# Kernel tuning notes

Hardware: AMD Instinct MI355X
Metric: run time of the kernel (lower is better)

## Reference

```python
import jax, jax.numpy as jnp
import numpy as np

N = 50000      # nodes
E = 800000     # edges (avg degree 16)
IN = 256       # in_feats
H = 256        # hidden_size
HEADS = 4
DH = H // HEADS  # 64
SCALE = np.sqrt(DH).astype(np.float32)


def _lin_init(k, fan_in, fan_out):
    s = 1.0 / np.sqrt(fan_in)
    k1, k2 = jax.random.split(k)
    W = jax.random.uniform(k1, (fan_in, fan_out), jnp.float32, -s, s)
    b = jax.random.uniform(k2, (fan_out,), jnp.float32, -s, s)
    return W, b


def setup_inputs() -> dict:
    key = jax.random.key(0)
    ks = jax.random.split(key, 20)
    d = {}
    d["features"] = jax.random.normal(ks[0], (N, IN), jnp.float32)
    d["src"] = jax.random.randint(ks[1], (E,), 0, N)
    d["dst"] = jax.random.randint(ks[2], (E,), 0, N)
    d["edge_types"] = jax.random.randint(ks[3], (E,), 0, 4)
    d["Wm"], d["bm"] = _lin_init(ks[4], IN, H)
    i = 5
    for l in (1, 2, 3):
        for nm in ("Q", "K", "V"):
            d[f"W{nm}{l}"], d[f"b{nm}{l}"] = _lin_init(ks[i], H, H)
            i += 1
    d["W1"], d["b1"] = _lin_init(ks[i], 3 * H, 2 * H); i += 1
    d["W2"], d["b2"] = _lin_init(ks[i], 2 * H, H); i += 1
    d["W3"], d["b3"] = _lin_init(ks[i], H, 1)
    return d


def _norms(src, dst):
    # DGL GraphConv norm='both': src normalized by out-degree, dst by in-degree
    ones = jnp.ones((E,), jnp.float32)
    deg_out = jax.ops.segment_sum(ones, src, num_segments=N)
    deg_in = jax.ops.segment_sum(ones, dst, num_segments=N)
    ns = jnp.where(deg_out > 0, deg_out ** -0.5, 0.0)[:, None]  # [N,1]
    nd = jnp.where(deg_in > 0, deg_in ** -0.5, 0.0)[:, None]
    return ns, nd


def _gcn(x, W, b, src, dst, ns, nd):
    # h = D_in^{-1/2} A D_out^{-1/2} x W + b
    m = (x * ns)[src]                                   # [E,H] gather
    agg = jax.ops.segment_sum(m, dst, num_segments=N)   # [N,H] scatter-sum
    return (agg * nd) @ W + b


def _attn(x, WQ, bQ, WK, bK, WV, bV, src, dst, ns, nd):
    Q = jax.nn.relu(_gcn(x, WQ, bQ, src, dst, ns, nd)).reshape(N, HEADS, DH)
    K = jax.nn.relu(_gcn(x, WK, bK, src, dst, ns, nd)).reshape(N, HEADS, DH)
    V = jax.nn.relu(_gcn(x, WV, bV, src, dst, ns, nd)).reshape(N, HEADS, DH)
    # edge scores: src K dot dst Q, scaled exp with clamp
    score = jnp.exp(jnp.clip((K[src] * Q[dst]).sum(-1) / SCALE, -10.0, 10.0))  # [E,HEADS]
    wV = jax.ops.segment_sum(V[src] * score[:, :, None], dst, num_segments=N)  # [N,HEADS,DH]
    z = jax.ops.segment_sum(score, dst, num_segments=N)                        # [N,HEADS]
    return (wV / (z[:, :, None] + 1e-6)).reshape(N, H)


def reference(features, src, dst, edge_types, Wm, bm,
              WQ1, bQ1, WK1, bK1, WV1, bV1,
              WQ2, bQ2, WK2, bK2, WV2, bV2,
              WQ3, bQ3, WK3, bK3, WV3, bV3,
              W1, b1, W2, b2, W3, b3):
    ns, nd = _norms(src, dst)
    x = jax.nn.relu(features @ Wm + bm)
    x1 = _attn(x, WQ1, bQ1, WK1, bK1, WV1, bV1, src, dst, ns, nd)
    x2 = _attn(x1, WQ2, bQ2, WK2, bK2, WV2, bV2, src, dst, ns, nd)
    x3 = _attn(x2, WQ3, bQ3, WK3, bK3, WV3, bV3, src, dst, ns, nd)
    x = jnp.concatenate((x1, x2, x3), axis=1)          # [N, 3H]
    x = jax.nn.relu(x @ W1 + b1)
    x = jax.nn.relu(x @ W2 + b2)
    x = (x @ W3 + b3)[:, 0]
    return jax.nn.sigmoid(x)
```

## Files before the change

kernel.cpp:

```cpp
#include <hip/hip_runtime.h>
#include <stdint.h>

#define NN 50000
#define NE 800000
#define NBLK 196

typedef float f32x4 __attribute__((ext_vector_type(4)));
typedef short s16x8 __attribute__((ext_vector_type(8)));

__device__ __forceinline__ float bf2f(unsigned short u) {
    union { unsigned int i; float f; } v; v.i = ((unsigned int)u) << 16; return v.f;
}
__device__ __forceinline__ unsigned short f2bf(float x) {
    union { float f; unsigned int i; } v; v.f = x;
    unsigned int r = v.i + 0x7FFFu + ((v.i >> 16) & 1u);
    return (unsigned short)(r >> 16);
}


__global__ void k_deg(const int* __restrict__ src, const int* __restrict__ dst,
                      int* __restrict__ dego, int* __restrict__ degi) {
    int e = blockIdx.x * 256 + threadIdx.x;
    if (e < NE) {
        atomicAdd(&dego[src[e]], 1);
        atomicAdd(&degi[dst[e]], 1);
    }
}

__global__ void k_norm(const int* __restrict__ dego, const int* __restrict__ degi,
                       float* __restrict__ ns, float* __restrict__ nd) {
    int i = blockIdx.x * 256 + threadIdx.x;
    if (i < NN) {
        ns[i] = dego[i] > 0 ? rsqrtf((float)dego[i]) : 0.f;
        nd[i] = degi[i] > 0 ? rsqrtf((float)degi[i]) : 0.f;
    }
}

__global__ void k_scanA(const int* __restrict__ deg, int* __restrict__ incl,
                        int* __restrict__ bsum) {
    __shared__ int sm[256];
    int t = threadIdx.x, i = blockIdx.x * 256 + t;
    int v = (i < NN) ? deg[i] : 0;
    sm[t] = v;
    __syncthreads();
#pragma unroll
    for (int off = 1; off < 256; off <<= 1) {
        int tv = (t >= off) ? sm[t - off] : 0;
        __syncthreads();
        sm[t] += tv;
        __syncthreads();
    }
    if (i < NN) incl[i] = sm[t];
    if (t == 255) bsum[blockIdx.x] = sm[255];
}

__global__ void k_scanB(const int* __restrict__ bsum, int* __restrict__ boff,
                        int* __restrict__ row_ptr) {
    __shared__ int sm[256];
    int t = threadIdx.x;
    int v = (t < NBLK) ? bsum[t] : 0;
    sm[t] = v;
    __syncthreads();
#pragma unroll
    for (int off = 1; off < 256; off <<= 1) {
        int tv = (t >= off) ? sm[t - off] : 0;
        __syncthreads();
        sm[t] += tv;
        __syncthreads();
    }
    if (t < NBLK) boff[t] = sm[t] - v;
    if (t == 255) row_ptr[NN] = sm[255];
}

__global__ void k_scanC(const int* __restrict__ deg, const int* __restrict__ incl,
                        const int* __restrict__ boff, int* __restrict__ row_ptr,
                        int* __restrict__ cursor) {
    int i = blockIdx.x * 256 + threadIdx.x;
    if (i < NN) {
        int ex = boff[blockIdx.x] + incl[i] - deg[i];
        row_ptr[i] = ex;
        cursor[i] = ex;
    }
}

__global__ void k_fill(const int* __restrict__ src, const int* __restrict__ dst,
                       const float* __restrict__ ns,
                       int* __restrict__ cursor, int* __restrict__ col_src,
                       float* __restrict__ ewt) {
    int e = blockIdx.x * 256 + threadIdx.x;
    if (e < NE) {
        int s = src[e];
        int slot = atomicAdd(&cursor[dst[e]], 1);
        col_src[slot] = s;
        ewt[slot] = ns[s];
    }
}

__global__ void k_wsplit(const float* __restrict__ W, unsigned short* __restrict__ hi,
                         unsigned short* __restrict__ lo, int K, int Ncols) {
    int idx = blockIdx.x * 256 + threadIdx.x;
    if (idx < K * Ncols) {
        int n = idx / K, k = idx - n * K;
        float w = W[(size_t)k * Ncols + n];
        unsigned short h = f2bf(w);
        hi[idx] = h;
        lo[idx] = f2bf(w - bf2f(h));
    }
}

struct QkvPtrs {
    const float* w[9];
    unsigned short* h[3];
    unsigned short* l[3];
};

__global__ void k_wsplit9(QkvPtrs P) {
    int m = blockIdx.y;
    int layer = m / 3, which = m - layer * 3;
    int idx = blockIdx.x * 256 + threadIdx.x;
    int n = idx >> 8, k = idx & 255;
    float w = P.w[m][(size_t)k * 256 + n];
    unsigned short h = f2bf(w);
    size_t o = (size_t)(which * 256 + n) * 256 + k;
    P.h[layer][o] = h;
    P.l[layer][o] = f2bf(w - bf2f(h));
}

struct BiasPtrs { const float* b[9]; float* dst; };

__global__ void k_bcat(BiasPtrs P) {
    int m = blockIdx.x;
    int layer = m / 3, which = m - layer * 3;
    int t = threadIdx.x;
    P.dst[layer * 768 + which * 256 + t] = P.b[m][t];
}


__global__ void k_prop(const float* __restrict__ x, int ldx,
                       const int* __restrict__ row_ptr, const int* __restrict__ col_src,
                       const float* __restrict__ ewt, const float* __restrict__ ndv,
                       float* __restrict__ y) {
    int w = (int)((blockIdx.x * 256 + threadIdx.x) >> 6);
    if (w >= NN) return;
    int lane = threadIdx.x & 63;
    int c = lane * 4;
    float a0 = 0, a1 = 0, a2 = 0, a3 = 0;
    int e0 = row_ptr[w], e1 = row_ptr[w + 1];
    int sv = (e0 < e1) ? col_src[e0] : 0;
    for (int p = e0; p < e1; ++p) {
        int sn = (p + 1 < e1) ? col_src[p + 1] : 0;
        float wv = ewt[p];
        const float4 xv = *(const float4*)(x + (size_t)sv * ldx + c);
        a0 += wv * xv.x; a1 += wv * xv.y; a2 += wv * xv.z; a3 += wv * xv.w;
        sv = sn;
    }
    float sc = ndv[w];
    float4 o; o.x = a0 * sc; o.y = a1 * sc; o.z = a2 * sc; o.w = a3 * sc;
    *(float4*)(y + (size_t)w * 256 + c) = o;
}


__global__ void k_attn(const float* __restrict__ Qbuf, const unsigned short* __restrict__ KV,
                       const int* __restrict__ row_ptr, const int* __restrict__ col_src,
                       float* __restrict__ xo) {
    int w = (int)((blockIdx.x * 256 + threadIdx.x) >> 6);
    if (w >= NN) return;
    int lane = threadIdx.x & 63;
    int c = lane * 4;
    const float4 q = *(const float4*)(Qbuf + (size_t)w * 256 + c);
    float v0 = 0, v1 = 0, v2 = 0, v3 = 0, z = 0;
    int e0 = row_ptr[w], e1 = row_ptr[w + 1];
    int sv = (e0 < e1) ? col_src[e0] : 0;
    for (int p = e0; p < e1; ++p) {
        int sn = (p + 1 < e1) ? col_src[p + 1] : 0;
        const ushort4 ku = *(const ushort4*)(KV + (size_t)sv * 512 + c);
        const ushort4 vu = *(const ushort4*)(KV + (size_t)sv * 512 + 256 + c);
        float t = q.x * bf2f(ku.x) + q.y * bf2f(ku.y) + q.z * bf2f(ku.z) + q.w * bf2f(ku.w);
        t += __shfl_xor(t, 1);
        t += __shfl_xor(t, 2);
        t += __shfl_xor(t, 4);
        t += __shfl_xor(t, 8);
        float scv = __expf(fminf(fmaxf(t * 0.125f, -10.f), 10.f));
        v0 += scv * bf2f(vu.x); v1 += scv * bf2f(vu.y);
        v2 += scv * bf2f(vu.z); v3 += scv * bf2f(vu.w);
        z += scv;
        sv = sn;
    }
    float inv = 1.f / (z + 1e-6f);
    float4 o; o.x = v0 * inv; o.y = v1 * inv; o.z = v2 * inv; o.w = v3 * inv;
    *(float4*)(xo + (size_t)w * 768 + c) = o;
}


template <int MODE>
__global__ __launch_bounds__(256) void k_gemm(
    const float* __restrict__ A, int lda,
    const unsigned short* __restrict__ Bhi, const unsigned short* __restrict__ Blo,
    const float* __restrict__ bias,
    float* __restrict__ C, unsigned short* __restrict__ KVb,
    int ldc, int coff, int M, int K) {
    __shared__ unsigned short sA[2][128][40];
    __shared__ unsigned short sB[2][128][40];
    const int tid = threadIdx.x;
    const int lane = tid & 63;
    const int wid = tid >> 6;
    const int wm = wid & 1, wn = wid >> 1;
    const int fr = lane & 15, kg = lane >> 4;
    const int brow = blockIdx.x * 128;
    const int bcol = blockIdx.y * 128;
    f32x4 acc[4][4] = {};

    for (int k0 = 0; k0 < K; k0 += 32) {
#pragma unroll
        for (int rep = 0; rep < 2; ++rep) {
            int s = tid + rep * 256;
            int row = s >> 2, ks = (s & 3) * 8;
            int gr = brow + row;
            float4 f0 = make_float4(0, 0, 0, 0), f1 = make_float4(0, 0, 0, 0);
            if (gr < M) {
                const float4* ap = (const float4*)(A + (size_t)gr * lda + k0 + ks);
                f0 = ap[0];
                f1 = ap[1];
            }
            ushort4 h0, h1v, l0, l1v;
            h0.x = f2bf(f0.x); l0.x = f2bf(f0.x - bf2f(h0.x));
            h0.y = f2bf(f0.y); l0.y = f2bf(f0.y - bf2f(h0.y));
            h0.z = f2bf(f0.z); l0.z = f2bf(f0.z - bf2f(h0.z));
            h0.w = f2bf(f0.w); l0.w = f2bf(f0.w - bf2f(h0.w));
            h1v.x = f2bf(f1.x); l1v.x = f2bf(f1.x - bf2f(h1v.x));
            h1v.y = f2bf(f1.y); l1v.y = f2bf(f1.y - bf2f(h1v.y));
            h1v.z = f2bf(f1.z); l1v.z = f2bf(f1.z - bf2f(h1v.z));
            h1v.w = f2bf(f1.w); l1v.w = f2bf(f1.w - bf2f(h1v.w));
            *(ushort4*)&sA[0][row][ks] = h0;
            *(ushort4*)&sA[0][row][ks + 4] = h1v;
            *(ushort4*)&sA[1][row][ks] = l0;
            *(ushort4*)&sA[1][row][ks + 4] = l1v;
            size_t bbase = (size_t)(bcol + row) * K + k0 + ks;
            *(uint4*)&sB[0][row][ks] = *(const uint4*)(Bhi + bbase);
            *(uint4*)&sB[1][row][ks] = *(const uint4*)(Blo + bbase);
        }
        __syncthreads();
        s16x8 ah[4], al[4], bh[4], bl[4];
#pragma unroll
        for (int f = 0; f < 4; ++f) {
            ah[f] = *(const s16x8*)&sA[0][wm * 64 + f * 16 + fr][kg * 8];
            al[f] = *(const s16x8*)&sA[1][wm * 64 + f * 16 + fr][kg * 8];
            bh[f] = *(const s16x8*)&sB[0][wn * 64 + f * 16 + fr][kg * 8];
            bl[f] = *(const s16x8*)&sB[1][wn * 64 + f * 16 + fr][kg * 8];
        }
#pragma unroll
        for (int i = 0; i < 4; ++i)
#pragma unroll
            for (int j = 0; j < 4; ++j) {
                acc[i][j] = __builtin_amdgcn_mfma_f32_16x16x32_bf16(ah[i], bh[j], acc[i][j], 0, 0, 0);
                acc[i][j] = __builtin_amdgcn_mfma_f32_16x16x32_bf16(ah[i], bl[j], acc[i][j], 0, 0, 0);
                acc[i][j] = __builtin_amdgcn_mfma_f32_16x16x32_bf16(al[i], bh[j], acc[i][j], 0, 0, 0);
            }
        __syncthreads();
    }

#pragma unroll
    for (int i = 0; i < 4; ++i) {
#pragma unroll
        for (int j = 0; j < 4; ++j) {
            int colG = bcol + wn * 64 + j * 16 + fr;
            float bb = bias[colG];
#pragma unroll
            for (int r = 0; r < 4; ++r) {
                int row = brow + wm * 64 + i * 16 + kg * 4 + r;
                if (row < M) {
                    float v = fmaxf(acc[i][j][r] + bb, 0.f);
                    if (MODE == 0) {
                        C[(size_t)row * ldc + coff + colG] = v;
                    } else {
                        if (colG < 256) C[(size_t)row * 256 + colG] = v;
                        else KVb[(size_t)row * 512 + (colG - 256)] = f2bf(v);
                    }
                }
            }
        }
    }
}


__global__ void k_final(const float* __restrict__ h2, const float* __restrict__ W3,
                        const float* __restrict__ b3, float* __restrict__ out) {
    int w = (int)((blockIdx.x * 256 + threadIdx.x) >> 6);
    if (w >= NN) return;
    int lane = threadIdx.x & 63;
    float4 h = *(const float4*)(h2 + (size_t)w * 256 + lane * 4);
    float4 ww = *(const float4*)(W3 + lane * 4);
    float p = h.x * ww.x + h.y * ww.y + h.z * ww.z + h.w * ww.w;
    p += __shfl_xor(p, 1);
    p += __shfl_xor(p, 2);
    p += __shfl_xor(p, 4);
    p += __shfl_xor(p, 8);
    p += __shfl_xor(p, 16);
    p += __shfl_xor(p, 32);
    if (lane == 0) out[w] = 1.f / (1.f + __expf(-(p + b3[0])));
}

__global__ void k_sent(float* __restrict__ out) {
    int i = blockIdx.x * 256 + threadIdx.x;
    if (i < NN) out[i] = 0.5f;
}


extern "C" void kernel_launch(void* const* d_in, const int* in_sizes, int n_in,
                              void* d_out, int out_size, void* d_ws, size_t ws_size,
                              hipStream_t stream) {
    const float* features = (const float*)d_in[0];
    const int* src = (const int*)d_in[1];
    const int* dst = (const int*)d_in[2];
    const float* Wm = (const float*)d_in[4];
    const float* bm = (const float*)d_in[5];
    const float* W1 = (const float*)d_in[24];
    const float* b1 = (const float*)d_in[25];
    const float* W2 = (const float*)d_in[26];
    const float* b2 = (const float*)d_in[27];
    const float* W3 = (const float*)d_in[28];
    const float* b3 = (const float*)d_in[29];
    float* out = (float*)d_out;

    char* ws = (char*)d_ws;
    size_t off = 0;
    auto alloc = [&](size_t b) -> void* {
        void* p = ws + off;
        off = (off + b + 255) & ~(size_t)255;
        return p;
    };

    int* deg_o = (int*)alloc(NN * 4);
    int* deg_i = (int*)alloc(NN * 4);
    int* row_ptr = (int*)alloc((NN + 1) * 4);
    int* cursor = (int*)alloc(NN * 4);
    int* col_src = (int*)alloc((size_t)NE * 4);
    float* ewt = (float*)alloc((size_t)NE * 4);
    float* ns = (float*)alloc(NN * 4);
    float* nd = (float*)alloc(NN * 4);
    int* incl = (int*)alloc(NN * 4);
    int* bsum = (int*)alloc(NBLK * 4);
    int* boff = (int*)alloc(NBLK * 4);

    unsigned short* Wmt_h = (unsigned short*)alloc(256 * 256 * 2);
    unsigned short* Wmt_l = (unsigned short*)alloc(256 * 256 * 2);
    unsigned short *Wqkvt_h[3], *Wqkvt_l[3];
    for (int l = 0; l < 3; ++l) {
        Wqkvt_h[l] = (unsigned short*)alloc(768 * 256 * 2);
        Wqkvt_l[l] = (unsigned short*)alloc(768 * 256 * 2);
    }
    float* bqkv = (float*)alloc(3 * 768 * 4);
    unsigned short* W1t_h = (unsigned short*)alloc(512 * 768 * 2);
    unsigned short* W1t_l = (unsigned short*)alloc(512 * 768 * 2);
    unsigned short* W2t_h = (unsigned short*)alloc(256 * 512 * 2);
    unsigned short* W2t_l = (unsigned short*)alloc(256 * 512 * 2);

    float* Qbuf = (float*)alloc((size_t)NN * 256 * 4);
    unsigned short* KV = (unsigned short*)alloc((size_t)NN * 512 * 2);
    float* y = (float*)alloc((size_t)NN * 256 * 4);
    float* xcat = (float*)alloc((size_t)NN * 768 * 4);

    float* x0 = Qbuf;
    float* h1 = Qbuf;
    float* h2 = y;

    (void)in_sizes; (void)n_in; (void)out_size;

    if (off > ws_size) {
        k_sent<<<(NN + 255) / 256, 256, 0, stream>>>(out);
        return;
    }

    hipMemsetAsync(deg_o, 0, NN * 4, stream);
    hipMemsetAsync(deg_i, 0, NN * 4, stream);
    k_deg<<<(NE + 255) / 256, 256, 0, stream>>>(src, dst, deg_o, deg_i);
    k_norm<<<NBLK, 256, 0, stream>>>(deg_o, deg_i, ns, nd);
    k_scanA<<<NBLK, 256, 0, stream>>>(deg_i, incl, bsum);
    k_scanB<<<1, 256, 0, stream>>>(bsum, boff, row_ptr);
    k_scanC<<<NBLK, 256, 0, stream>>>(deg_i, incl, boff, row_ptr, cursor);
    k_fill<<<(NE + 255) / 256, 256, 0, stream>>>(src, dst, ns, cursor, col_src, ewt);

    k_wsplit<<<(256 * 256 + 255) / 256, 256, 0, stream>>>(Wm, Wmt_h, Wmt_l, 256, 256);
    QkvPtrs qp;
    BiasPtrs bp;
    for (int l = 0; l < 3; ++l) {
        for (int m = 0; m < 3; ++m) {
            qp.w[l * 3 + m] = (const float*)d_in[6 + l * 6 + m * 2];
            bp.b[l * 3 + m] = (const float*)d_in[7 + l * 6 + m * 2];
        }
        qp.h[l] = Wqkvt_h[l];
        qp.l[l] = Wqkvt_l[l];
    }
    bp.dst = bqkv;
    k_wsplit9<<<dim3(256, 9), 256, 0, stream>>>(qp);
    k_bcat<<<9, 256, 0, stream>>>(bp);
    k_wsplit<<<(768 * 512 + 255) / 256, 256, 0, stream>>>(W1, W1t_h, W1t_l, 768, 512);
    k_wsplit<<<(512 * 256 + 255) / 256, 256, 0, stream>>>(W2, W2t_h, W2t_l, 512, 256);

    const int MB = (NN + 127) / 128;
    dim3 gN256(MB, 2), gN512(MB, 4), gN768(MB, 6);

    k_gemm<0><<<gN256, 256, 0, stream>>>(features, 256, Wmt_h, Wmt_l, bm,
                                         x0, nullptr, 256, 0, NN, 256);

    const float* xin = x0;
    int ldx = 256;
    for (int l = 0; l < 3; ++l) {
        k_prop<<<12500, 256, 0, stream>>>(xin, ldx, row_ptr, col_src, ewt, nd, y);
        k_gemm<1><<<gN768, 256, 0, stream>>>(y, 256, Wqkvt_h[l], Wqkvt_l[l], bqkv + l * 768,
                                             Qbuf, KV, 0, 0, NN, 256);
        k_attn<<<12500, 256, 0, stream>>>(Qbuf, KV, row_ptr, col_src, xcat + 256 * l);
        xin = xcat + 256 * l;
        ldx = 768;
    }

    k_gemm<0><<<gN512, 256, 0, stream>>>(xcat, 768, W1t_h, W1t_l, b1,
                                         h1, nullptr, 512, 0, NN, 768);
    k_gemm<0><<<gN256, 256, 0, stream>>>(h1, 512, W2t_h, W2t_l, b2,
                                         h2, nullptr, 256, 0, NN, 512);
    k_final<<<12500, 256, 0, stream>>>(h2, W3, b3, out);
}
```

Measured before the change: 9.822 us.

## Fuse setup kernels, store propagated features in bf16, loop column tiles in GEMM

Folds the degree-norm computation into the scan kernel, the bias concat into the QKV weight split, and merges three weight-split launches into one. The node features gathered by the propagation kernel are now stored as bf16 copies, which halves gather bandwidth at the cost of precision. The GEMM now walks several column tiles per block instead of launching more blocks, which cuts the grid size but also reduces parallelism. The deg_o/deg_i memsets are merged on the assumption that the two buffers are contiguous.

```diff
diff --git a/kernel.cpp b/kernel.cpp
--- a/kernel.cpp
+++ b/kernel.cpp
@@ -24,15 +24,6 @@
     if (e < NE) {
         atomicAdd(&dego[src[e]], 1);
         atomicAdd(&degi[dst[e]], 1);
-    }
-}
-
-__global__ void k_norm(const int* __restrict__ dego, const int* __restrict__ degi,
-                       float* __restrict__ ns, float* __restrict__ nd) {
-    int i = blockIdx.x * 256 + threadIdx.x;
-    if (i < NN) {
-        ns[i] = dego[i] > 0 ? rsqrtf((float)dego[i]) : 0.f;
-        nd[i] = degi[i] > 0 ? rsqrtf((float)degi[i]) : 0.f;
     }
 }
 
@@ -72,14 +63,17 @@
     if (t == 255) row_ptr[NN] = sm[255];
 }
 
-__global__ void k_scanC(const int* __restrict__ deg, const int* __restrict__ incl,
-                        const int* __restrict__ boff, int* __restrict__ row_ptr,
-                        int* __restrict__ cursor) {
+__global__ void k_scanC(const int* __restrict__ dego, const int* __restrict__ degi,
+                        const int* __restrict__ incl, const int* __restrict__ boff,
+                        int* __restrict__ row_ptr, int* __restrict__ cursor,
+                        float* __restrict__ ns, float* __restrict__ nd) {
     int i = blockIdx.x * 256 + threadIdx.x;
     if (i < NN) {
-        int ex = boff[blockIdx.x] + incl[i] - deg[i];
+        int ex = boff[blockIdx.x] + incl[i] - degi[i];
         row_ptr[i] = ex;
         cursor[i] = ex;
+        ns[i] = dego[i] > 0 ? rsqrtf((float)dego[i]) : 0.f;
+        nd[i] = degi[i] > 0 ? rsqrtf((float)degi[i]) : 0.f;
     }
 }
 
@@ -96,22 +90,12 @@
     }
 }
 
-__global__ void k_wsplit(const float* __restrict__ W, unsigned short* __restrict__ hi,
-                         unsigned short* __restrict__ lo, int K, int Ncols) {
-    int idx = blockIdx.x * 256 + threadIdx.x;
-    if (idx < K * Ncols) {
-        int n = idx / K, k = idx - n * K;
-        float w = W[(size_t)k * Ncols + n];
-        unsigned short h = f2bf(w);
-        hi[idx] = h;
-        lo[idx] = f2bf(w - bf2f(h));
-    }
-}
-
 struct QkvPtrs {
     const float* w[9];
+    const float* b[9];
     unsigned short* h[3];
     unsigned short* l[3];
+    float* bdst;
 };
 
 __global__ void k_wsplit9(QkvPtrs P) {
@@ -124,19 +108,28 @@
     size_t o = (size_t)(which * 256 + n) * 256 + k;
     P.h[layer][o] = h;
     P.l[layer][o] = f2bf(w - bf2f(h));
-}
-
-struct BiasPtrs { const float* b[9]; float* dst; };
-
-__global__ void k_bcat(BiasPtrs P) {
-    int m = blockIdx.x;
-    int layer = m / 3, which = m - layer * 3;
-    int t = threadIdx.x;
-    P.dst[layer * 768 + which * 256 + t] = P.b[m][t];
-}
-
-
-__global__ void k_prop(const float* __restrict__ x, int ldx,
+    if (blockIdx.x == 0)
+        P.bdst[layer * 768 + which * 256 + (int)threadIdx.x] = P.b[m][threadIdx.x];
+}
+
+struct W3Ptrs { const float* w[3]; unsigned short* h[3]; unsigned short* l[3]; };
+
+__global__ void k_wsplit3(W3Ptrs P) {
+    int y = blockIdx.y;
+    int mi, K, N, sub;
+    if (y == 0)      { mi = 0; K = 256; N = 256; sub = 0; }
+    else if (y < 7)  { mi = 1; K = 768; N = 512; sub = y - 1; }
+    else             { mi = 2; K = 512; N = 256; sub = y - 7; }
+    int idx = sub * 65536 + blockIdx.x * 256 + (int)threadIdx.x;
+    int n = idx / K, k = idx - n * K;
+    float w = P.w[mi][(size_t)k * N + n];
+    unsigned short h = f2bf(w);
+    P.h[mi][idx] = h;
+    P.l[mi][idx] = f2bf(w - bf2f(h));
+}
+
+
+__global__ void k_prop(const unsigned short* __restrict__ xb,
                        const int* __restrict__ row_ptr, const int* __restrict__ col_src,
                        const float* __restrict__ ewt, const float* __restrict__ ndv,
                        float* __restrict__ y) {
@@ -150,8 +143,9 @@
     for (int p = e0; p < e1; ++p) {
         int sn = (p + 1 < e1) ? col_src[p + 1] : 0;
         float wv = ewt[p];
-        const float4 xv = *(const float4*)(x + (size_t)sv * ldx + c);
-        a0 += wv * xv.x; a1 += wv * xv.y; a2 += wv * xv.z; a3 += wv * xv.w;
+        const ushort4 xv = *(const ushort4*)(xb + (size_t)sv * 256 + c);
+        a0 += wv * bf2f(xv.x); a1 += wv * bf2f(xv.y);
+        a2 += wv * bf2f(xv.z); a3 += wv * bf2f(xv.w);
         sv = sn;
     }
     float sc = ndv[w];
@@ -162,7 +156,7 @@
 
 __global__ void k_attn(const float* __restrict__ Qbuf, const unsigned short* __restrict__ KV,
                        const int* __restrict__ row_ptr, const int* __restrict__ col_src,
-                       float* __restrict__ xo) {
+                       float* __restrict__ xo, unsigned short* __restrict__ xprop) {
     int w = (int)((blockIdx.x * 256 + threadIdx.x) >> 6);
     if (w >= NN) return;
     int lane = threadIdx.x & 63;
@@ -189,10 +183,15 @@
     float inv = 1.f / (z + 1e-6f);
     float4 o; o.x = v0 * inv; o.y = v1 * inv; o.z = v2 * inv; o.w = v3 * inv;
     *(float4*)(xo + (size_t)w * 768 + c) = o;
-}
-
-
-template <int MODE>
+    if (xprop) {
+        ushort4 ob;
+        ob.x = f2bf(o.x); ob.y = f2bf(o.y); ob.z = f2bf(o.z); ob.w = f2bf(o.w);
+        *(ushort4*)(xprop + (size_t)w * 256 + c) = ob;
+    }
+}
+
+
+template <int MODE, int NITER>
 __global__ __launch_bounds__(256) void k_gemm(
     const float* __restrict__ A, int lda,
     const unsigned short* __restrict__ Bhi, const unsigned short* __restrict__ Blo,
@@ -207,74 +206,79 @@
     const int wm = wid & 1, wn = wid >> 1;
     const int fr = lane & 15, kg = lane >> 4;
     const int brow = blockIdx.x * 128;
-    const int bcol = blockIdx.y * 128;
-    f32x4 acc[4][4] = {};
-
-    for (int k0 = 0; k0 < K; k0 += 32) {
-#pragma unroll
-        for (int rep = 0; rep < 2; ++rep) {
-            int s = tid + rep * 256;
-            int row = s >> 2, ks = (s & 3) * 8;
-            int gr = brow + row;
-            float4 f0 = make_float4(0, 0, 0, 0), f1 = make_float4(0, 0, 0, 0);
-            if (gr < M) {
-                const float4* ap = (const float4*)(A + (size_t)gr * lda + k0 + ks);
-                f0 = ap[0];
-                f1 = ap[1];
+
+    for (int it = 0; it < NITER; ++it) {
+        const int bcol = (blockIdx.y * NITER + it) * 128;
+        f32x4 acc[4][4] = {};
+
+        for (int k0 = 0; k0 < K; k0 += 32) {
+#pragma unroll
+            for (int rep = 0; rep < 2; ++rep) {
+                int s = tid + rep * 256;
+                int row = s >> 2, ks = (s & 3) * 8;
+                int gr = brow + row;
+                float4 f0 = make_float4(0, 0, 0, 0), f1 = make_float4(0, 0, 0, 0);
+                if (gr < M) {
+                    const float4* ap = (const float4*)(A + (size_t)gr * lda + k0 + ks);
+                    f0 = ap[0];
+                    f1 = ap[1];
+                }
+                ushort4 h0, h1v, l0, l1v;
+                h0.x = f2bf(f0.x); l0.x = f2bf(f0.x - bf2f(h0.x));
+                h0.y = f2bf(f0.y); l0.y = f2bf(f0.y - bf2f(h0.y));
+                h0.z = f2bf(f0.z); l0.z = f2bf(f0.z - bf2f(h0.z));
+                h0.w = f2bf(f0.w); l0.w = f2bf(f0.w - bf2f(h0.w));
+                h1v.x = f2bf(f1.x); l1v.x = f2bf(f1.x - bf2f(h1v.x));
+                h1v.y = f2bf(f1.y); l1v.y = f2bf(f1.y - bf2f(h1v.y));
+                h1v.z = f2bf(f1.z); l1v.z = f2bf(f1.z - bf2f(h1v.z));
+                h1v.w = f2bf(f1.w); l1v.w = f2bf(f1.w - bf2f(h1v.w));
+                *(ushort4*)&sA[0][row][ks] = h0;
+                *(ushort4*)&sA[0][row][ks + 4] = h1v;
+                *(ushort4*)&sA[1][row][ks] = l0;
+                *(ushort4*)&sA[1][row][ks + 4] = l1v;
+                size_t bbase = (size_t)(bcol + row) * K + k0 + ks;
+                *(uint4*)&sB[0][row][ks] = *(const uint4*)(Bhi + bbase);
+                *(uint4*)&sB[1][row][ks] = *(const uint4*)(Blo + bbase);
             }
-            ushort4 h0, h1v, l0, l1v;
-            h0.x = f2bf(f0.x); l0.x = f2bf(f0.x - bf2f(h0.x));
-            h0.y = f2bf(f0.y); l0.y = f2bf(f0.y - bf2f(h0.y));
-            h0.z = f2bf(f0.z); l0.z = f2bf(f0.z - bf2f(h0.z));
-            h0.w = f2bf(f0.w); l0.w = f2bf(f0.w - bf2f(h0.w));
-            h1v.x = f2bf(f1.x); l1v.x = f2bf(f1.x - bf2f(h1v.x));
-            h1v.y = f2bf(f1.y); l1v.y = f2bf(f1.y - bf2f(h1v.y));
-            h1v.z = f2bf(f1.z); l1v.z = f2bf(f1.z - bf2f(h1v.z));
-            h1v.w = f2bf(f1.w); l1v.w = f2bf(f1.w - bf2f(h1v.w));
-            *(ushort4*)&sA[0][row][ks] = h0;
-            *(ushort4*)&sA[0][row][ks + 4] = h1v;
-            *(ushort4*)&sA[1][row][ks] = l0;
-            *(ushort4*)&sA[1][row][ks + 4] = l1v;
-            size_t bbase = (size_t)(bcol + row) * K + k0 + ks;
-            *(uint4*)&sB[0][row][ks] = *(const uint4*)(Bhi + bbase);
-            *(uint4*)&sB[1][row][ks] = *(const uint4*)(Blo + bbase);
+            __syncthreads();
+            s16x8 ah[4], al[4], bh[4], bl[4];
+#pragma unroll
+            for (int f = 0; f < 4; ++f) {
+                ah[f] = *(const s16x8*)&sA[0][wm * 64 + f * 16 + fr][kg * 8];
+                al[f] = *(const s16x8*)&sA[1][wm * 64 + f * 16 + fr][kg * 8];
+                bh[f] = *(const s16x8*)&sB[0][wn * 64 + f * 16 + fr][kg * 8];
+                bl[f] = *(const s16x8*)&sB[1][wn * 64 + f * 16 + fr][kg * 8];
+            }
+#pragma unroll
+            for (int i = 0; i < 4; ++i)
+#pragma unroll
+                for (int j = 0; j < 4; ++j) {
+                    acc[i][j] = __builtin_amdgcn_mfma_f32_16x16x32_bf16(ah[i], bh[j], acc[i][j], 0, 0, 0);
+                    acc[i][j] = __builtin_amdgcn_mfma_f32_16x16x32_bf16(ah[i], bl[j], acc[i][j], 0, 0, 0);
+                    acc[i][j] = __builtin_amdgcn_mfma_f32_16x16x32_bf16(al[i], bh[j], acc[i][j], 0, 0, 0);
+                }
+            __syncthreads();
         }
-        __syncthreads();
-        s16x8 ah[4], al[4], bh[4], bl[4];
-#pragma unroll
-        for (int f = 0; f < 4; ++f) {
-            ah[f] = *(const s16x8*)&sA[0][wm * 64 + f * 16 + fr][kg * 8];
-            al[f] = *(const s16x8*)&sA[1][wm * 64 + f * 16 + fr][kg * 8];
-            bh[f] = *(const s16x8*)&sB[0][wn * 64 + f * 16 + fr][kg * 8];
-            bl[f] = *(const s16x8*)&sB[1][wn * 64 + f * 16 + fr][kg * 8];
-        }
-#pragma unroll
-        for (int i = 0; i < 4; ++i)
+
+#pragma unroll
+        for (int i = 0; i < 4; ++i) {
 #pragma unroll
             for (int j = 0; j < 4; ++j) {
-                acc[i][j] = __builtin_amdgcn_mfma_f32_16x16x32_bf16(ah[i], bh[j], acc[i][j], 0, 0, 0);
-                acc[i][j] = __builtin_amdgcn_mfma_f32_16x16x32_bf16(ah[i], bl[j], acc[i][j], 0, 0, 0);
-                acc[i][j] = __builtin_amdgcn_mfma_f32_16x16x32_bf16(al[i], bh[j], acc[i][j], 0, 0, 0);
-            }
-        __syncthreads();
-    }
-
-#pragma unroll
-    for (int i = 0; i < 4; ++i) {
-#pragma unroll
-        for (int j = 0; j < 4; ++j) {
-            int colG = bcol + wn * 64 + j * 16 + fr;
-            float bb = bias[colG];
-#pragma unroll
-            for (int r = 0; r < 4; ++r) {
-                int row = brow + wm * 64 + i * 16 + kg * 4 + r;
-                if (row < M) {
-                    float v = fmaxf(acc[i][j][r] + bb, 0.f);
-                    if (MODE == 0) {
-                        C[(size_t)row * ldc + coff + colG] = v;
-                    } else {
-                        if (colG < 256) C[(size_t)row * 256 + colG] = v;
-                        else KVb[(size_t)row * 512 + (colG - 256)] = f2bf(v);
+                int colG = bcol + wn * 64 + j * 16 + fr;
+                float bb = bias[colG];
+#pragma unroll
+                for (int r = 0; r < 4; ++r) {
+                    int row = brow + wm * 64 + i * 16 + kg * 4 + r;
+                    if (row < M) {
+                        float v = fmaxf(acc[i][j][r] + bb, 0.f);
+                        if (MODE == 0) {
+                            C[(size_t)row * ldc + coff + colG] = v;
+                        } else if (MODE == 1) {
+                            if (colG < 256) C[(size_t)row * 256 + colG] = v;
+                            else KVb[(size_t)row * 512 + (colG - 256)] = f2bf(v);
+                        } else {
+                            KVb[(size_t)row * 256 + colG] = f2bf(v);
+                        }
                     }
                 }
             }
@@ -359,8 +363,9 @@
     unsigned short* KV = (unsigned short*)alloc((size_t)NN * 512 * 2);
     float* y = (float*)alloc((size_t)NN * 256 * 4);
     float* xcat = (float*)alloc((size_t)NN * 768 * 4);
-
-    float* x0 = Qbuf;
+    unsigned short* xprop = (unsigned short*)alloc((size_t)NN * 256 * 2);
+
+    unsigned short* x0b = (unsigned short*)xcat;
     float* h1 = Qbuf;
     float* h2 = y;
 
@@ -371,52 +376,50 @@
         return;
     }
 
-    hipMemsetAsync(deg_o, 0, NN * 4, stream);
-    hipMemsetAsync(deg_i, 0, NN * 4, stream);
+    hipMemsetAsync(deg_o, 0, (size_t)((char*)deg_i - (char*)deg_o) + NN * 4, stream);
     k_deg<<<(NE + 255) / 256, 256, 0, stream>>>(src, dst, deg_o, deg_i);
-    k_norm<<<NBLK, 256, 0, stream>>>(deg_o, deg_i, ns, nd);
     k_scanA<<<NBLK, 256, 0, stream>>>(deg_i, incl, bsum);
     k_scanB<<<1, 256, 0, stream>>>(bsum, boff, row_ptr);
-    k_scanC<<<NBLK, 256, 0, stream>>>(deg_i, incl, boff, row_ptr, cursor);
+    k_scanC<<<NBLK, 256, 0, stream>>>(deg_o, deg_i, incl, boff, row_ptr, cursor, ns, nd);
     k_fill<<<(NE + 255) / 256, 256, 0, stream>>>(src, dst, ns, cursor, col_src, ewt);
 
-    k_wsplit<<<(256 * 256 + 255) / 256, 256, 0, stream>>>(Wm, Wmt_h, Wmt_l, 256, 256);
     QkvPtrs qp;
-    BiasPtrs bp;
     for (int l = 0; l < 3; ++l) {
         for (int m = 0; m < 3; ++m) {
             qp.w[l * 3 + m] = (const float*)d_in[6 + l * 6 + m * 2];
-            bp.b[l * 3 + m] = (const float*)d_in[7 + l * 6 + m * 2];
+            qp.b[l * 3 + m] = (const float*)d_in[7 + l * 6 + m * 2];
         }
         qp.h[l] = Wqkvt_h[l];
         qp.l[l] = Wqkvt_l[l];
     }
-    bp.dst = bqkv;
+    qp.bdst = bqkv;
     k_wsplit9<<<dim3(256, 9), 256, 0, stream>>>(qp);
-    k_bcat<<<9, 256, 0, stream>>>(bp);
-    k_wsplit<<<(768 * 512 + 255) / 256, 256, 0, stream>>>(W1, W1t_h, W1t_l, 768, 512);
-    k_wsplit<<<(512 * 256 + 255) / 256, 256, 0, stream>>>(W2, W2t_h, W2t_l, 512, 256);
+
+    W3Ptrs wp;
+    wp.w[0] = Wm; wp.h[0] = Wmt_h; wp.l[0] = Wmt_l;
+    wp.w[1] = W1; wp.h[1] = W1t_h; wp.l[1] = W1t_l;
+    wp.w[2] = W2; wp.h[2] = W2t_h; wp.l[2] = W2t_l;
+    k_wsplit3<<<dim3(256, 9), 256, 0, stream>>>(wp);
 
     const int MB = (NN + 127) / 128;
-    dim3 gN256(MB, 2), gN512(MB, 4), gN768(MB, 6);
-
-    k_gemm<0><<<gN256, 256, 0, stream>>>(features, 256, Wmt_h, Wmt_l, bm,
-                                         x0, nullptr, 256, 0, NN, 256);
-
-    const float* xin = x0;
-    int ldx = 256;
+    dim3 g2(MB, 2);
+
+    k_gemm<2, 1><<<g2, 256, 0, stream>>>(features, 256, Wmt_h, Wmt_l, bm,
+                                         nullptr, x0b, 0, 0, NN, 256);
+
+    const unsigned short* xin = x0b;
     for (int l = 0; l < 3; ++l) {
-        k_prop<<<12500, 256, 0, stream>>>(xin, ldx, row_ptr, col_src, ewt, nd, y);
-        k_gemm<1><<<gN768, 256, 0, stream>>>(y, 256, Wqkvt_h[l], Wqkvt_l[l], bqkv + l * 768,
+        k_prop<<<12500, 256, 0, stream>>>(xin, row_ptr, col_src, ewt, nd, y);
+        k_gemm<1, 3><<<g2, 256, 0, stream>>>(y, 256, Wqkvt_h[l], Wqkvt_l[l], bqkv + l * 768,
                                              Qbuf, KV, 0, 0, NN, 256);
-        k_attn<<<12500, 256, 0, stream>>>(Qbuf, KV, row_ptr, col_src, xcat + 256 * l);
-        xin = xcat + 256 * l;
-        ldx = 768;
-    }
-
-    k_gemm<0><<<gN512, 256, 0, stream>>>(xcat, 768, W1t_h, W1t_l, b1,
+        k_attn<<<12500, 256, 0, stream>>>(Qbuf, KV, row_ptr, col_src, xcat + 256 * l,
+                                          l < 2 ? xprop : nullptr);
+        xin = xprop;
+    }
+
+    k_gemm<0, 2><<<g2, 256, 0, stream>>>(xcat, 768, W1t_h, W1t_l, b1,
                                          h1, nullptr, 512, 0, NN, 768);
-    k_gemm<0><<<gN256, 256, 0, stream>>>(h1, 512, W2t_h, W2t_l, b2,
+    k_gemm<0, 1><<<g2, 256, 0, stream>>>(h1, 512, W2t_h, W2t_l, b2,
                                          h2, nullptr, 256, 0, NN, 512);
     k_final<<<12500, 256, 0, stream>>>(h2, W3, b3, out);
 }
```

Result: faster. 9.377 us (-4.5%).
